# Kernel optimization log

Measured on AMD Instinct MI355X. Metric: run time of the kernel, lower is better.

The kernel has to match this reference:

```python
import jax, jax.numpy as jnp
import numpy as np

NBINS = 256
STRENGTH = 100.0  # __init__ strength kwarg


def _hist_channel(x):
    # x: [N] flattened masked channel -> 256-bin histogram over [min,max]
    lo = jnp.min(x)
    hi = jnp.max(x)
    scale = (NBINS - 1) / jnp.maximum(hi - lo, 1e-12)
    bins = jnp.clip(jnp.floor((x - lo) * scale + 0.5).astype(jnp.int32), 0, NBINS - 1)
    return jnp.zeros((NBINS,), dtype=x.dtype).at[bins].add(1.0)


def _match_channel(x, t_hist):
    # CDF-based histogram matching (cpp.matchHistogram): remap sorted values of x
    # to bin centers of the target histogram; output normalized to [0,1].
    N = x.shape[0]
    idx = jnp.argsort(x)
    t = t_hist * (N / jnp.maximum(jnp.sum(t_hist), 1e-12))
    cdf = jnp.cumsum(t)  # [NBINS]
    ranks = jnp.arange(N, dtype=cdf.dtype) + 0.5
    bins = jnp.clip(jnp.searchsorted(cdf, ranks), 0, NBINS - 1)
    vals = bins.astype(x.dtype) / (NBINS - 1)
    return jnp.zeros_like(x).at[idx].set(vals)


def reference(input, masks, target_hists, target_mins, target_maxs):
    # input: [1,C,H,W]; masks: [S,H,W]; target_hists: [S,C,256]; mins/maxs: [S,C]
    C = input.shape[1]
    x = input[0]  # [C,H,W]

    def per_style(mask, t_hist, t_min, t_max):
        mf = (x * mask[None]).reshape(C, -1)  # masked feature, [C,N]
        hist = jax.vmap(_hist_channel)(mf)    # computed every call (as in source)
        matched = jax.vmap(_match_channel)(mf, t_hist)  # [C,N] in [0,1]
        target = matched * (t_max - t_min)[:, None] + t_min[:, None]
        target = jax.lax.stop_gradient(target)  # torch uses .data (detached)
        loss = 0.01 * STRENGTH * jnp.mean((mf - target) ** 2)  # nn.MSELoss
        return loss, hist

    losses, hists = jax.vmap(per_style)(masks, target_hists, target_mins, target_maxs)
    return jnp.sum(losses), hists


def setup_inputs() -> dict:
    key = jax.random.key(0)
    k1, k2, k3, k4 = jax.random.split(key, 4)
    S, C, H, W = 2, 256, 256, 256
    input = jax.random.normal(k1, (1, C, H, W), dtype=jnp.float32)
    masks = (jax.random.uniform(k2, (S, H, W)) > 0.5).astype(jnp.float32)
    target_hists = jax.random.uniform(k3, (S, C, NBINS), dtype=jnp.float32) * 100.0
    base = jax.random.normal(k4, (S, C), dtype=jnp.float32)
    target_mins = base - 1.0
    target_maxs = base + 1.0
    return {"input": input, "masks": masks, "target_hists": target_hists,
            "target_mins": target_mins, "target_maxs": target_maxs}
```

## Files before the change

### kernel.cpp

```cpp
#include <hip/hip_runtime.h>
#include <math.h>

#define NBINS 256
#define NB    4096

__global__ void mask_bits_kernel(const float* __restrict__ masks,
                                 unsigned* __restrict__ bits, int total)
{
    const int idx = blockIdx.x * blockDim.x + threadIdx.x;
    bool m = false;
    if (idx < total) m = (masks[idx] != 0.0f);
    const unsigned long long b = __ballot(m);
    const int lane = threadIdx.x & 63;
    if (idx < total) {
        if (lane == 0)       bits[idx >> 5] = (unsigned)b;
        else if (lane == 32) bits[idx >> 5] = (unsigned)(b >> 32);
    }
}

__device__ inline void stat4(float4 xv, unsigned w,
                             float& vmin, float& vmax, float& ssq, float& zc)
{
    const float v0 = (w & 1u) ? xv.x : 0.0f;
    const float v1 = (w & 2u) ? xv.y : 0.0f;
    const float v2 = (w & 4u) ? xv.z : 0.0f;
    const float v3 = (w & 8u) ? xv.w : 0.0f;
    vmin = fminf(vmin, fminf(fminf(v0, v1), fminf(v2, v3)));
    vmax = fmaxf(vmax, fmaxf(fmaxf(v0, v1), fmaxf(v2, v3)));
    ssq += v0 * v0 + v1 * v1 + v2 * v2 + v3 * v3;
    zc += (v0 == 0.0f ? 1.0f : 0.0f) + (v1 == 0.0f ? 1.0f : 0.0f)
        + (v2 == 0.0f ? 1.0f : 0.0f) + (v3 == 0.0f ? 1.0f : 0.0f);
}

__device__ inline void bin4(float4 xv, unsigned w, float lo, float sc16,
                            unsigned* __restrict__ cnt)
{
    const float e[4] = { (w & 1u) ? xv.x : 0.0f, (w & 2u) ? xv.y : 0.0f,
                         (w & 4u) ? xv.z : 0.0f, (w & 8u) ? xv.w : 0.0f };
    #pragma unroll
    for (int j = 0; j < 4; ++j) {
        const float v = e[j];
        if (v != 0.0f) {
            const int jb = min(NB - 1, max(0, (int)floorf((v - lo) * sc16 + 8.0f)));
            atomicAdd(&cnt[jb], 1u);
        }
    }
}

__global__ __launch_bounds__(1024, 4) void fused_kernel(
    const float* __restrict__ x, const unsigned* __restrict__ bits,
    const float* __restrict__ thist, const float* __restrict__ tmins,
    const float* __restrict__ tmaxs,
    float* __restrict__ out, float* __restrict__ lossws, int C, int N)
{
    const int c = blockIdx.x;
    const float* __restrict__ xc = x + (size_t)c * N;
    const unsigned* __restrict__ wb0 = bits;
    const unsigned* __restrict__ wb1 = bits + (N >> 5);
    const int tid = threadIdx.x, lane = tid & 63, wid = tid >> 6;

    __shared__ unsigned cntS[2][2][NB + 1];
    __shared__ float Sarr[2][NBINS];
    __shared__ int   Karr[2][NBINS];
    __shared__ float thsum[2][4];
    __shared__ unsigned ctot[16];
    __shared__ float wtot[16];
    __shared__ float lsum[16];
    __shared__ float stats8[2][4];
    __shared__ float wr[8][16];

    float mn0 = 3.4e38f, mx0 = -3.4e38f, sq0 = 0.f, z0 = 0.f;
    float mn1 = 3.4e38f, mx1 = -3.4e38f, sq1 = 0.f, z1 = 0.f;
    const int step = 1024 * 4;
    int i = tid * 4;
    for (; i + 3 * step < N; i += 4 * step) {
        float4 xv[4]; unsigned w0[4], w1[4];
        #pragma unroll
        for (int q = 0; q < 4; ++q) {
            const int ii = i + q * step;
            xv[q] = *reinterpret_cast<const float4*>(xc + ii);
            w0[q] = wb0[ii >> 5] >> (ii & 31);
            w1[q] = wb1[ii >> 5] >> (ii & 31);
        }
        #pragma unroll
        for (int q = 0; q < 4; ++q) {
            stat4(xv[q], w0[q], mn0, mx0, sq0, z0);
            stat4(xv[q], w1[q], mn1, mx1, sq1, z1);
        }
    }
    for (; i < N; i += step) {
        const float4 xv = *reinterpret_cast<const float4*>(xc + i);
        stat4(xv, wb0[i >> 5] >> (i & 31), mn0, mx0, sq0, z0);
        stat4(xv, wb1[i >> 5] >> (i & 31), mn1, mx1, sq1, z1);
    }
    #pragma unroll
    for (int off = 32; off > 0; off >>= 1) {
        mn0 = fminf(mn0, __shfl_xor(mn0, off));
        mx0 = fmaxf(mx0, __shfl_xor(mx0, off));
        sq0 += __shfl_xor(sq0, off);
        z0  += __shfl_xor(z0, off);
        mn1 = fminf(mn1, __shfl_xor(mn1, off));
        mx1 = fmaxf(mx1, __shfl_xor(mx1, off));
        sq1 += __shfl_xor(sq1, off);
        z1  += __shfl_xor(z1, off);
    }
    if (lane == 0) {
        wr[0][wid] = mn0; wr[1][wid] = mx0; wr[2][wid] = sq0; wr[3][wid] = z0;
        wr[4][wid] = mn1; wr[5][wid] = mx1; wr[6][wid] = sq1; wr[7][wid] = z1;
    }

    const int g  = tid >> 8;
    const int gi = tid & 255;
    const int gw = (tid >> 6) & 3;
    float th = 0.f, thscan = 0.f;
    if (g < 2) {
        th = thist[(size_t)(g * C + c) * NBINS + gi];
        thscan = th;
        #pragma unroll
        for (int off = 1; off < 64; off <<= 1) {
            const float t = __shfl_up(thscan, off);
            if (lane >= off) thscan += t;
        }
        if (lane == 63) thsum[g][gw] = thscan;
    }
    {
        unsigned* cf = &cntS[0][0][0];
        for (int k = tid; k < 2 * 2 * (NB + 1); k += 1024) cf[k] = 0u;
    }
    __syncthreads();

    if (tid < 2) {
        const int b8 = tid * 4;
        float mn = wr[b8 + 0][0], mx = wr[b8 + 1][0];
        float sq = wr[b8 + 2][0], z = wr[b8 + 3][0];
        for (int k = 1; k < 16; ++k) {
            mn = fminf(mn, wr[b8 + 0][k]); mx = fmaxf(mx, wr[b8 + 1][k]);
            sq += wr[b8 + 2][k]; z += wr[b8 + 3][k];
        }
        stats8[tid][0] = mn; stats8[tid][1] = mx; stats8[tid][2] = sq; stats8[tid][3] = z;
    }
    __syncthreads();

    const float lo0 = stats8[0][0], rng0 = fmaxf(stats8[0][1] - lo0, 1e-12f);
    const float lo1 = stats8[1][0], rng1 = fmaxf(stats8[1][1] - lo1, 1e-12f);
    const float sc16_0 = 4080.0f / rng0;
    const float sc16_1 = 4080.0f / rng1;

    if (g < 2) {
        float cross = 0.f, tsum = 0.f;
        #pragma unroll
        for (int w2 = 0; w2 < 4; ++w2) { if (w2 < gw) cross += thsum[g][w2]; tsum += thsum[g][w2]; }
        const float scale = (float)N / fmaxf(tsum, 1e-12f);
        const float cdfv = (thscan + cross) * scale;
        int K = (int)floorf(cdfv - 0.5f) + 1;
        K = min(N, max(0, K));
        if (gi == NBINS - 1) K = N;
        Karr[g][gi] = K;
    }

    const int copy = wid >> 3;
    unsigned* __restrict__ c0 = cntS[0][copy];
    unsigned* __restrict__ c1 = cntS[1][copy];
    i = tid * 4;
    for (; i + 3 * step < N; i += 4 * step) {
        float4 xv[4]; unsigned w0[4], w1[4];
        #pragma unroll
        for (int q = 0; q < 4; ++q) {
            const int ii = i + q * step;
            xv[q] = *reinterpret_cast<const float4*>(xc + ii);
            w0[q] = wb0[ii >> 5] >> (ii & 31);
            w1[q] = wb1[ii >> 5] >> (ii & 31);
        }
        #pragma unroll
        for (int q = 0; q < 4; ++q) {
            bin4(xv[q], w0[q], lo0, sc16_0, c0);
            bin4(xv[q], w1[q], lo1, sc16_1, c1);
        }
    }
    for (; i < N; i += step) {
        const float4 xv = *reinterpret_cast<const float4*>(xc + i);
        bin4(xv, wb0[i >> 5] >> (i & 31), lo0, sc16_0, c0);
        bin4(xv, wb1[i >> 5] >> (i & 31), lo1, sc16_1, c1);
    }
    __syncthreads();

    const int st = tid >> 9;
    const int t  = tid & 511;
    const int b8 = t * 8;
    unsigned c_[8]; float w_[8];
    unsigned csum = 0u; float wsum = 0.f;
    #pragma unroll
    for (int q = 0; q < 8; ++q) {
        c_[q] = cntS[st][0][b8 + q] + cntS[st][1][b8 + q];
        w_[q] = (float)c_[q] * ((float)(b8 + q) - 7.5f);
        csum += c_[q]; wsum += w_[q];
    }
    unsigned cin = csum; float win = wsum;
    #pragma unroll
    for (int off = 1; off < 64; off <<= 1) {
        const unsigned cu = __shfl_up(cin, off);
        const float    wu = __shfl_up(win, off);
        if (lane >= off) { cin += cu; win += wu; }
    }
    if (lane == 63) { ctot[wid] = cin; wtot[wid] = win; }
    __syncthreads();
    unsigned cofs = 0u; float wofs = 0.f;
    #pragma unroll
    for (int w2 = 0; w2 < 16; ++w2)
        if (w2 >= st * 8 && w2 < wid) { cofs += ctot[w2]; wofs += wtot[w2]; }
    unsigned cex = cofs + (cin - csum);
    float    wex = wofs + (win - wsum);
    {
        unsigned* __restrict__ cp = cntS[st][0];
        float*    __restrict__ WF = (float*)cntS[st][1];
        #pragma unroll
        for (int q = 0; q < 8; ++q) {
            cp[b8 + q] = cex; WF[b8 + q] = wex;
            cex += c_[q]; wex += w_[q];
        }
        if (t == 511) { cp[NB] = cex; WF[NB] = wex; }
    }
    __syncthreads();

    if (g < 2) {
        const float lo  = stats8[g][0];
        const float rng = fmaxf(stats8[g][1] - lo, 1e-12f);
        const float sc16 = 4080.0f / rng;
        const float u    = rng / 4080.0f;
        const float schist = 255.0f / rng;
        const unsigned n0 = (unsigned)stats8[g][3];
        const int ib0 = min(NBINS - 1, max(0, (int)floorf((0.0f - lo) * schist + 0.5f)));
        const int b0  = min(NB - 1,    max(0, (int)floorf((0.0f - lo) * sc16 + 8.0f)));
        unsigned* __restrict__ cp = cntS[g][0];
        float*    __restrict__ WF = (float*)cntS[g][1];

        unsigned h = cp[16 * gi + 16] - cp[16 * gi];
        if (gi == ib0) h += n0;
        out[1 + (size_t)(g * C + c) * NBINS + gi] = (float)h;

        const unsigned Z0 = cp[b0];
        const unsigned k = (unsigned)Karr[g][gi];
        float Sv;
        if (gi == NBINS - 1) {
            Sv = lo * (float)cp[NB] + u * WF[NB];
        } else if (k <= Z0) {
            int jlo = 0, jhi = b0;
            while (jlo < jhi) { const int mid = (jlo + jhi + 1) >> 1;
                if (cp[mid] <= k) jlo = mid; else jhi = mid - 1; }
            const unsigned d = k - cp[jlo];
            Sv = lo * (float)k + u * (WF[jlo] + (float)d * ((float)jlo - 7.5f));
        } else if (k <= Z0 + n0) {
            Sv = lo * (float)Z0 + u * WF[b0];
        } else {
            const unsigned k2 = k - n0;
            int jlo = b0, jhi = NB;
            while (jlo < jhi) { const int mid = (jlo + jhi + 1) >> 1;
                if (cp[mid] <= k2) jlo = mid; else jhi = mid - 1; }
            const unsigned d = k2 - cp[jlo];
            Sv = lo * (float)k2 + u * (WF[jlo] + (float)d * ((float)jlo - 7.5f));
        }
        Sarr[g][gi] = Sv;
    }
    __syncthreads();

    float term = 0.f;
    if (g < 2) {
        const float tmn = tmins[g * C + c], tmx = tmaxs[g * C + c];
        const float Tb = ((float)gi / 255.0f) * (tmx - tmn) + tmn;
        const float Sb = Sarr[g][gi];
        const float Sp = (gi == 0) ? 0.f : Sarr[g][gi - 1];
        const int   Kb = Karr[g][gi];
        const int   Kp = (gi == 0) ? 0 : Karr[g][gi - 1];
        term = -2.0f * Tb * (Sb - Sp) + Tb * Tb * (float)(Kb - Kp);
    }
    #pragma unroll
    for (int off = 32; off > 0; off >>= 1) term += __shfl_xor(term, off);
    if (lane == 0) lsum[wid] = term;
    __syncthreads();
    if (tid == 0) {
        const float t0 = (lsum[0] + lsum[1]) + (lsum[2] + lsum[3]);
        const float t1 = (lsum[4] + lsum[5]) + (lsum[6] + lsum[7]);
        const float inv = 1.0f / ((float)C * (float)N);
        lossws[c]     = (stats8[0][2] + t0) * inv;
        lossws[C + c] = (stats8[1][2] + t1) * inv;
    }
}

__global__ void reduce_loss_kernel(const float* __restrict__ lossws,
                                   float* __restrict__ out, int n)
{
    __shared__ float sh[256];
    const int tid = threadIdx.x;
    float v = 0.f;
    for (int i = tid; i < n; i += 256) v += lossws[i];
    sh[tid] = v;
    __syncthreads();
    for (int st = 128; st > 0; st >>= 1) {
        if (tid < st) sh[tid] += sh[tid + st];
        __syncthreads();
    }
    if (tid == 0) out[0] = sh[0];
}

extern "C" void kernel_launch(void* const* d_in, const int* in_sizes, int n_in,
                              void* d_out, int out_size, void* d_ws, size_t ws_size,
                              hipStream_t stream)
{
    const float* x     = (const float*)d_in[0];
    const float* masks = (const float*)d_in[1];
    const float* thist = (const float*)d_in[2];
    const float* tmins = (const float*)d_in[3];
    const float* tmaxs = (const float*)d_in[4];
    float* out = (float*)d_out;

    const int SC = in_sizes[3];
    const long long ratio = (long long)in_sizes[0] / (long long)in_sizes[1];
    const long long csq   = (long long)SC * ratio;
    const int C = (int)(sqrt((double)csq) + 0.5);
    const int S = SC / C;
    const int N = in_sizes[1] / S;
    const int total = in_sizes[1];

    float* lossws = (float*)d_ws;
    const size_t off1 = ((size_t)SC * 4 + 255) & ~(size_t)255;
    unsigned* bits = (unsigned*)((char*)d_ws + off1);

    mask_bits_kernel<<<(total + 1023) / 1024, 1024, 0, stream>>>(masks, bits, total);
    fused_kernel<<<C, 1024, 0, stream>>>(x, bits, thist, tmins, tmaxs,
                                         out, lossws, C, N);
    reduce_loss_kernel<<<1, 256, 0, stream>>>(lossws, out, SC);
}
```

Measured before the change: 43.76 us.

## Load 32 contiguous elements per thread, drop zero counting, use four histogram copies

Each thread now handles 32 contiguous elements per iteration, so one mask word serves 32 values instead of being reloaded for each float4. The explicit zero-count statistic is removed and recovered as N minus the total binned count. Binning now tests the mask bit directly instead of checking for a nonzero value, and the shared-memory histogram is split into four copies instead of two to reduce atomic contention. The cost is more LDS use (about 131KB for counts), which may limit occupancy, and larger per-thread register arrays.

```diff
diff --git a/kernel.cpp b/kernel.cpp
--- a/kernel.cpp
+++ b/kernel.cpp
@@ -3,6 +3,7 @@
 
 #define NBINS 256
 #define NB    4096
+#define NCOPY 4
 
 __global__ void mask_bits_kernel(const float* __restrict__ masks,
                                  unsigned* __restrict__ bits, int total)
@@ -18,35 +19,6 @@
     }
 }
 
-__device__ inline void stat4(float4 xv, unsigned w,
-                             float& vmin, float& vmax, float& ssq, float& zc)
-{
-    const float v0 = (w & 1u) ? xv.x : 0.0f;
-    const float v1 = (w & 2u) ? xv.y : 0.0f;
-    const float v2 = (w & 4u) ? xv.z : 0.0f;
-    const float v3 = (w & 8u) ? xv.w : 0.0f;
-    vmin = fminf(vmin, fminf(fminf(v0, v1), fminf(v2, v3)));
-    vmax = fmaxf(vmax, fmaxf(fmaxf(v0, v1), fmaxf(v2, v3)));
-    ssq += v0 * v0 + v1 * v1 + v2 * v2 + v3 * v3;
-    zc += (v0 == 0.0f ? 1.0f : 0.0f) + (v1 == 0.0f ? 1.0f : 0.0f)
-        + (v2 == 0.0f ? 1.0f : 0.0f) + (v3 == 0.0f ? 1.0f : 0.0f);
-}
-
-__device__ inline void bin4(float4 xv, unsigned w, float lo, float sc16,
-                            unsigned* __restrict__ cnt)
-{
-    const float e[4] = { (w & 1u) ? xv.x : 0.0f, (w & 2u) ? xv.y : 0.0f,
-                         (w & 4u) ? xv.z : 0.0f, (w & 8u) ? xv.w : 0.0f };
-    #pragma unroll
-    for (int j = 0; j < 4; ++j) {
-        const float v = e[j];
-        if (v != 0.0f) {
-            const int jb = min(NB - 1, max(0, (int)floorf((v - lo) * sc16 + 8.0f)));
-            atomicAdd(&cnt[jb], 1u);
-        }
-    }
-}
-
 __global__ __launch_bounds__(1024, 4) void fused_kernel(
     const float* __restrict__ x, const unsigned* __restrict__ bits,
     const float* __restrict__ thist, const float* __restrict__ tmins,
@@ -59,7 +31,7 @@
     const unsigned* __restrict__ wb1 = bits + (N >> 5);
     const int tid = threadIdx.x, lane = tid & 63, wid = tid >> 6;
 
-    __shared__ unsigned cntS[2][2][NB + 1];
+    __shared__ unsigned cntS[2][NCOPY][NB + 1];
     __shared__ float Sarr[2][NBINS];
     __shared__ int   Karr[2][NBINS];
     __shared__ float thsum[2][4];
@@ -67,46 +39,59 @@
     __shared__ float wtot[16];
     __shared__ float lsum[16];
     __shared__ float stats8[2][4];
-    __shared__ float wr[8][16];
-
-    float mn0 = 3.4e38f, mx0 = -3.4e38f, sq0 = 0.f, z0 = 0.f;
-    float mn1 = 3.4e38f, mx1 = -3.4e38f, sq1 = 0.f, z1 = 0.f;
-    const int step = 1024 * 4;
-    int i = tid * 4;
-    for (; i + 3 * step < N; i += 4 * step) {
-        float4 xv[4]; unsigned w0[4], w1[4];
-        #pragma unroll
-        for (int q = 0; q < 4; ++q) {
-            const int ii = i + q * step;
-            xv[q] = *reinterpret_cast<const float4*>(xc + ii);
-            w0[q] = wb0[ii >> 5] >> (ii & 31);
-            w1[q] = wb1[ii >> 5] >> (ii & 31);
-        }
-        #pragma unroll
-        for (int q = 0; q < 4; ++q) {
-            stat4(xv[q], w0[q], mn0, mx0, sq0, z0);
-            stat4(xv[q], w1[q], mn1, mx1, sq1, z1);
-        }
-    }
-    for (; i < N; i += step) {
+    __shared__ float wr[6][16];
+
+    const int step32 = 1024 * 32;
+    const int Nmain  = (N / step32) * step32;
+
+    float mn0 = 3.4e38f, mx0 = -3.4e38f, sq0 = 0.f;
+    float mn1 = 3.4e38f, mx1 = -3.4e38f, sq1 = 0.f;
+    for (int i = tid * 32; i < Nmain; i += step32) {
+        float4 a[8];
+        #pragma unroll
+        for (int q = 0; q < 8; ++q)
+            a[q] = *reinterpret_cast<const float4*>(xc + i + q * 4);
+        const unsigned w0 = wb0[i >> 5];
+        const unsigned w1 = wb1[i >> 5];
+        #pragma unroll
+        for (int q = 0; q < 8; ++q) {
+            const float e[4] = { a[q].x, a[q].y, a[q].z, a[q].w };
+            #pragma unroll
+            for (int el = 0; el < 4; ++el) {
+                const int j = q * 4 + el;
+                const float xv = e[el];
+                const float v0 = ((w0 >> j) & 1u) ? xv : 0.0f;
+                const float v1 = ((w1 >> j) & 1u) ? xv : 0.0f;
+                mn0 = fminf(mn0, v0); mx0 = fmaxf(mx0, v0); sq0 += v0 * v0;
+                mn1 = fminf(mn1, v1); mx1 = fmaxf(mx1, v1); sq1 += v1 * v1;
+            }
+        }
+    }
+    for (int i = Nmain + tid * 4; i < N; i += 1024 * 4) {
         const float4 xv = *reinterpret_cast<const float4*>(xc + i);
-        stat4(xv, wb0[i >> 5] >> (i & 31), mn0, mx0, sq0, z0);
-        stat4(xv, wb1[i >> 5] >> (i & 31), mn1, mx1, sq1, z1);
+        const unsigned w0 = wb0[i >> 5] >> (i & 31);
+        const unsigned w1 = wb1[i >> 5] >> (i & 31);
+        const float e[4] = { xv.x, xv.y, xv.z, xv.w };
+        #pragma unroll
+        for (int j = 0; j < 4; ++j) {
+            const float v0 = ((w0 >> j) & 1u) ? e[j] : 0.0f;
+            const float v1 = ((w1 >> j) & 1u) ? e[j] : 0.0f;
+            mn0 = fminf(mn0, v0); mx0 = fmaxf(mx0, v0); sq0 += v0 * v0;
+            mn1 = fminf(mn1, v1); mx1 = fmaxf(mx1, v1); sq1 += v1 * v1;
+        }
     }
     #pragma unroll
     for (int off = 32; off > 0; off >>= 1) {
         mn0 = fminf(mn0, __shfl_xor(mn0, off));
         mx0 = fmaxf(mx0, __shfl_xor(mx0, off));
         sq0 += __shfl_xor(sq0, off);
-        z0  += __shfl_xor(z0, off);
         mn1 = fminf(mn1, __shfl_xor(mn1, off));
         mx1 = fmaxf(mx1, __shfl_xor(mx1, off));
         sq1 += __shfl_xor(sq1, off);
-        z1  += __shfl_xor(z1, off);
     }
     if (lane == 0) {
-        wr[0][wid] = mn0; wr[1][wid] = mx0; wr[2][wid] = sq0; wr[3][wid] = z0;
-        wr[4][wid] = mn1; wr[5][wid] = mx1; wr[6][wid] = sq1; wr[7][wid] = z1;
+        wr[0][wid] = mn0; wr[1][wid] = mx0; wr[2][wid] = sq0;
+        wr[3][wid] = mn1; wr[4][wid] = mx1; wr[5][wid] = sq1;
     }
 
     const int g  = tid >> 8;
@@ -125,19 +110,18 @@
     }
     {
         unsigned* cf = &cntS[0][0][0];
-        for (int k = tid; k < 2 * 2 * (NB + 1); k += 1024) cf[k] = 0u;
+        for (int k = tid; k < 2 * NCOPY * (NB + 1); k += 1024) cf[k] = 0u;
     }
     __syncthreads();
 
     if (tid < 2) {
-        const int b8 = tid * 4;
-        float mn = wr[b8 + 0][0], mx = wr[b8 + 1][0];
-        float sq = wr[b8 + 2][0], z = wr[b8 + 3][0];
+        const int b6 = tid * 3;
+        float mn = wr[b6 + 0][0], mx = wr[b6 + 1][0], sq = wr[b6 + 2][0];
         for (int k = 1; k < 16; ++k) {
-            mn = fminf(mn, wr[b8 + 0][k]); mx = fmaxf(mx, wr[b8 + 1][k]);
-            sq += wr[b8 + 2][k]; z += wr[b8 + 3][k];
-        }
-        stats8[tid][0] = mn; stats8[tid][1] = mx; stats8[tid][2] = sq; stats8[tid][3] = z;
+            mn = fminf(mn, wr[b6 + 0][k]); mx = fmaxf(mx, wr[b6 + 1][k]);
+            sq += wr[b6 + 2][k];
+        }
+        stats8[tid][0] = mn; stats8[tid][1] = mx; stats8[tid][2] = sq;
     }
     __syncthreads();
 
@@ -158,29 +142,50 @@
         Karr[g][gi] = K;
     }
 
-    const int copy = wid >> 3;
+    const int copy = wid >> 2;
     unsigned* __restrict__ c0 = cntS[0][copy];
     unsigned* __restrict__ c1 = cntS[1][copy];
-    i = tid * 4;
-    for (; i + 3 * step < N; i += 4 * step) {
-        float4 xv[4]; unsigned w0[4], w1[4];
-        #pragma unroll
-        for (int q = 0; q < 4; ++q) {
-            const int ii = i + q * step;
-            xv[q] = *reinterpret_cast<const float4*>(xc + ii);
-            w0[q] = wb0[ii >> 5] >> (ii & 31);
-            w1[q] = wb1[ii >> 5] >> (ii & 31);
-        }
-        #pragma unroll
-        for (int q = 0; q < 4; ++q) {
-            bin4(xv[q], w0[q], lo0, sc16_0, c0);
-            bin4(xv[q], w1[q], lo1, sc16_1, c1);
-        }
-    }
-    for (; i < N; i += step) {
+    for (int i = tid * 32; i < Nmain; i += step32) {
+        float4 a[8];
+        #pragma unroll
+        for (int q = 0; q < 8; ++q)
+            a[q] = *reinterpret_cast<const float4*>(xc + i + q * 4);
+        const unsigned w0 = wb0[i >> 5];
+        const unsigned w1 = wb1[i >> 5];
+        #pragma unroll
+        for (int q = 0; q < 8; ++q) {
+            const float e[4] = { a[q].x, a[q].y, a[q].z, a[q].w };
+            #pragma unroll
+            for (int el = 0; el < 4; ++el) {
+                const int j = q * 4 + el;
+                const float xv = e[el];
+                if ((w0 >> j) & 1u) {
+                    const int jb = min(NB - 1, max(0, (int)floorf((xv - lo0) * sc16_0 + 8.0f)));
+                    atomicAdd(&c0[jb], 1u);
+                }
+                if ((w1 >> j) & 1u) {
+                    const int jb = min(NB - 1, max(0, (int)floorf((xv - lo1) * sc16_1 + 8.0f)));
+                    atomicAdd(&c1[jb], 1u);
+                }
+            }
+        }
+    }
+    for (int i = Nmain + tid * 4; i < N; i += 1024 * 4) {
         const float4 xv = *reinterpret_cast<const float4*>(xc + i);
-        bin4(xv, wb0[i >> 5] >> (i & 31), lo0, sc16_0, c0);
-        bin4(xv, wb1[i >> 5] >> (i & 31), lo1, sc16_1, c1);
+        const unsigned w0 = wb0[i >> 5] >> (i & 31);
+        const unsigned w1 = wb1[i >> 5] >> (i & 31);
+        const float e[4] = { xv.x, xv.y, xv.z, xv.w };
+        #pragma unroll
+        for (int j = 0; j < 4; ++j) {
+            if ((w0 >> j) & 1u) {
+                const int jb = min(NB - 1, max(0, (int)floorf((e[j] - lo0) * sc16_0 + 8.0f)));
+                atomicAdd(&c0[jb], 1u);
+            }
+            if ((w1 >> j) & 1u) {
+                const int jb = min(NB - 1, max(0, (int)floorf((e[j] - lo1) * sc16_1 + 8.0f)));
+                atomicAdd(&c1[jb], 1u);
+            }
+        }
     }
     __syncthreads();
 
@@ -191,9 +196,12 @@
     unsigned csum = 0u; float wsum = 0.f;
     #pragma unroll
     for (int q = 0; q < 8; ++q) {
-        c_[q] = cntS[st][0][b8 + q] + cntS[st][1][b8 + q];
-        w_[q] = (float)c_[q] * ((float)(b8 + q) - 7.5f);
-        csum += c_[q]; wsum += w_[q];
+        unsigned cc = cntS[st][0][b8 + q];
+        #pragma unroll
+        for (int cp2 = 1; cp2 < NCOPY; ++cp2) cc += cntS[st][cp2][b8 + q];
+        c_[q] = cc;
+        w_[q] = (float)cc * ((float)(b8 + q) - 7.5f);
+        csum += cc; wsum += w_[q];
     }
     unsigned cin = csum; float win = wsum;
     #pragma unroll
@@ -228,11 +236,11 @@
         const float sc16 = 4080.0f / rng;
         const float u    = rng / 4080.0f;
         const float schist = 255.0f / rng;
-        const unsigned n0 = (unsigned)stats8[g][3];
+        unsigned* __restrict__ cp = cntS[g][0];
+        float*    __restrict__ WF = (float*)cntS[g][1];
+        const unsigned n0 = (unsigned)N - cp[NB];
         const int ib0 = min(NBINS - 1, max(0, (int)floorf((0.0f - lo) * schist + 0.5f)));
         const int b0  = min(NB - 1,    max(0, (int)floorf((0.0f - lo) * sc16 + 8.0f)));
-        unsigned* __restrict__ cp = cntS[g][0];
-        float*    __restrict__ WF = (float*)cntS[g][1];
 
         unsigned h = cp[16 * gi + 16] - cp[16 * gi];
         if (gi == ib0) h += n0;
```

Measured after the change: 43.93 us. No clear change (+0.4%).
